# Kernel optimization log

Measured on AMD Instinct MI355X. Metric: run time of the kernel, lower is better.

Reference implementation:

```python
import jax, jax.numpy as jnp
import numpy as np

TEMP = 0.05
ALPHA = 0.1
EPS = 1e-12


def setup_inputs() -> dict:
    key = jax.random.key(0)
    k1, k2, k3, k4 = jax.random.split(key, 4)
    bs, emb_dim, n_class, n_aux = 16384, 512, 2000, 5
    features = jax.random.normal(k1, (bs, emb_dim), dtype=jnp.float32)
    word_embed = jax.random.normal(k2, (n_class, emb_dim), dtype=jnp.float32)
    label = jax.random.randint(k3, (bs,), 0, n_class)
    aux = jax.random.randint(k4, (bs, n_aux), 0, n_class)
    return {"features": features, "word_embed": word_embed, "label": label, "aux": aux}


def _cosine_logits(features, word_embed):
    # F.normalize(x, dim=-1): x / max(||x||, eps)
    f = features / jnp.maximum(jnp.linalg.norm(features, axis=-1, keepdims=True), EPS)
    w = word_embed / jnp.maximum(jnp.linalg.norm(word_embed, axis=-1, keepdims=True), EPS)
    return jnp.matmul(f, w.T) / TEMP  # (bs, n_class)


def reference(features, word_embed, label, aux):
    pred = _cosine_logits(features, word_embed)
    lse = jax.nn.logsumexp(pred, axis=1)                                  # log sum exp per row
    tgt = jnp.take_along_axis(pred, label[:, None], axis=1)[:, 0]         # pred[i, target[i]]
    # normal cross entropy: mean_i(-pred[i,t_i] + log sum exp(pred[i]))
    loss_normal = jnp.mean(-tgt + lse)
    # label-smoothing CE: -(1-a)*pred[i,t_i] + lse - (a/n_aux)*sum_j pred[i, aux[i,j]]
    single_alpha = ALPHA / aux.shape[-1]
    aux_logits = jnp.take_along_axis(pred, aux, axis=1)                   # (bs, n_aux)
    loss_ls = jnp.mean(-(1.0 - ALPHA) * tgt + lse - single_alpha * jnp.sum(aux_logits, axis=1))
    loss = 0.5 * (loss_normal + loss_ls)
    acc = jnp.mean((jnp.argmax(pred, axis=1) == label).astype(jnp.float32))
    return loss, acc
```

## Files before the change

kernel.cpp:

```cpp
#include <hip/hip_runtime.h>
#include <hip/hip_bf16.h>
#include <stdint.h>

#define BS   16384
#define NC   2000
#define NCP  2048
#define EMB  512
#define NAUX 5
#define NCHUNK 32
#define GBLK 4096

typedef __bf16 bf16x8 __attribute__((ext_vector_type(8)));
typedef float  f32x4  __attribute__((ext_vector_type(4)));

__global__ __launch_bounds__(256) void norm_kernel(
    const float* __restrict__ feat, const float* __restrict__ wemb,
    __bf16* __restrict__ fn, __bf16* __restrict__ wn)
{
    const int sub = threadIdx.x & 15;
    const int row = blockIdx.x * 16 + (threadIdx.x >> 4);

    if (row >= BS + NC) {
        bf16x8 z = {};
        bf16x8* d = (bf16x8*)(wn + (size_t)(row - BS) * EMB) + sub * 4;
        #pragma unroll
        for (int i = 0; i < 4; ++i) d[i] = z;
        return;
    }
    const float* src;
    __bf16* dst;
    if (row < BS) { src = feat + (size_t)row * EMB;        dst = fn + (size_t)row * EMB; }
    else          { src = wemb + (size_t)(row - BS) * EMB; dst = wn + (size_t)(row - BS) * EMB; }

    const float4* s4 = (const float4*)src + sub * 8;
    float4 x[8];
    float ss = 0.f;
    #pragma unroll
    for (int i = 0; i < 8; ++i) {
        x[i] = s4[i];
        ss += x[i].x * x[i].x + x[i].y * x[i].y + x[i].z * x[i].z + x[i].w * x[i].w;
    }
    #pragma unroll
    for (int m = 1; m < 16; m <<= 1) ss += __shfl_xor(ss, m, 64);
    const float scale = 1.0f / fmaxf(sqrtf(ss), 1e-12f);

    bf16x8* d = (bf16x8*)dst + sub * 4;
    #pragma unroll
    for (int i = 0; i < 4; ++i) {
        bf16x8 o;
        o[0] = (__bf16)(x[2*i].x   * scale); o[1] = (__bf16)(x[2*i].y   * scale);
        o[2] = (__bf16)(x[2*i].z   * scale); o[3] = (__bf16)(x[2*i].w   * scale);
        o[4] = (__bf16)(x[2*i+1].x * scale); o[5] = (__bf16)(x[2*i+1].y * scale);
        o[6] = (__bf16)(x[2*i+1].z * scale); o[7] = (__bf16)(x[2*i+1].w * scale);
        d[i] = o;
    }
}

__global__ __launch_bounds__(256) void main_kernel(
    const __bf16* __restrict__ fn, const __bf16* __restrict__ wn,
    float* __restrict__ es_p, unsigned* __restrict__ key_p)
{
    __shared__ __align__(16) __bf16 As[128 * 64];
    __shared__ __align__(16) __bf16 Bs[128 * 64];

    const int tid   = threadIdx.x;
    const int lane  = tid & 63;
    const int l15   = lane & 15;
    const int quad  = lane >> 4;
    const int wv    = tid >> 6;
    const int wvM   = wv >> 1;
    const int wvN   = wv & 1;
    const int xcd   = blockIdx.x & 7;
    const int j     = blockIdx.x >> 3;
    const int mTile = xcd * 16 + (j >> 4);
    const int nTile = j & 15;

    const __bf16* fbase = fn + (size_t)mTile * 128 * EMB;
    const __bf16* wbase = wn + (size_t)nTile * 128 * EMB;

    const int sRowIn = lane >> 3;
    const int sChunk = (lane & 7) ^ sRowIn;
    f32x4 acc[4][4] = {};

    for (int kk = 0; kk < EMB; kk += 64) {
        __syncthreads();
        #pragma unroll
        for (int p = 0; p < 4; ++p) {
            const int slot = wv * 4 + p;
            const size_t goff = (size_t)(slot * 8 + sRowIn) * EMB + kk + sChunk * 8;
            __builtin_amdgcn_global_load_lds(
                (const __attribute__((address_space(1))) void*)(fbase + goff),
                (__attribute__((address_space(3))) void*)(As + slot * 512), 16, 0, 0);
            __builtin_amdgcn_global_load_lds(
                (const __attribute__((address_space(1))) void*)(wbase + goff),
                (__attribute__((address_space(3))) void*)(Bs + slot * 512), 16, 0, 0);
        }
        __builtin_amdgcn_s_waitcnt(0);
        __syncthreads();

        #pragma unroll
        for (int kc = 0; kc < 2; ++kc) {
            bf16x8 aF[4], bF[4];
            #pragma unroll
            for (int i = 0; i < 4; ++i) {
                const int ar = wvM * 64 + i * 16 + l15;
                const int br = wvN * 64 + i * 16 + l15;
                const int ca = ((kc * 4 + quad) ^ (ar & 7)) * 8;
                const int cb = ((kc * 4 + quad) ^ (br & 7)) * 8;
                aF[i] = *(const bf16x8*)(As + ar * 64 + ca);
                bF[i] = *(const bf16x8*)(Bs + br * 64 + cb);
            }
            #pragma unroll
            for (int mi = 0; mi < 4; ++mi)
                #pragma unroll
                for (int ni = 0; ni < 4; ++ni)
                    acc[mi][ni] = __builtin_amdgcn_mfma_f32_16x16x32_bf16(
                        aF[mi], bF[ni], acc[mi][ni], 0, 0, 0);
        }
    }

    const float C20 = 28.853900817779268f;
    const int chunk = nTile * 2 + wvN;
    #pragma unroll
    for (int mi = 0; mi < 4; ++mi) {
        float    es[4] = {0.f, 0.f, 0.f, 0.f};
        unsigned km[4] = {0u, 0u, 0u, 0u};
        #pragma unroll
        for (int ni = 0; ni < 4; ++ni) {
            const int col = nTile * 128 + wvN * 64 + ni * 16 + l15;
            const unsigned colenc = 2047u - (unsigned)col;
            const bool valid = (col < NC);
            #pragma unroll
            for (int r = 0; r < 4; ++r) {
                float v = valid ? acc[mi][ni][r] : -3.0f;
                es[r] += exp2f((v - 1.0f) * C20);
                unsigned u = __float_as_uint(v);
                unsigned k = u ^ (unsigned)(((int)u >> 31) | 0x80000000);
                unsigned pk = (k & 0xFFFFF800u) | colenc;
                km[r] = pk > km[r] ? pk : km[r];
            }
        }
        #pragma unroll
        for (int r = 0; r < 4; ++r) {
            #pragma unroll
            for (int m = 1; m < 16; m <<= 1) {
                es[r] += __shfl_xor(es[r], m, 64);
                unsigned x = __shfl_xor(km[r], m, 64);
                km[r] = x > km[r] ? x : km[r];
            }
        }
        if (l15 == 0) {
            #pragma unroll
            for (int r = 0; r < 4; ++r) {
                const int row = mTile * 128 + wvM * 64 + mi * 16 + quad * 4 + r;
                es_p [(size_t)row * NCHUNK + chunk] = es[r];
                key_p[(size_t)row * NCHUNK + chunk] = km[r];
            }
        }
    }
}

__global__ __launch_bounds__(256) void gather_fin_kernel(
    const __bf16* __restrict__ fn, const __bf16* __restrict__ wn,
    const int* __restrict__ label, const int* __restrict__ aux,
    const float* __restrict__ es_p, const unsigned* __restrict__ key_p,
    float* __restrict__ blkpart)
{
    const int lane = threadIdx.x & 63;
    const int wv   = threadIdx.x >> 6;
    const int row  = blockIdx.x * 4 + wv;

    bf16x8 f8 = *((const bf16x8*)fn + (size_t)row * (EMB / 8) + lane);
    float fv[8];
    #pragma unroll
    for (int j = 0; j < 8; ++j) fv[j] = (float)f8[j];

    const int lab = label[row];
    int cols[6];
    cols[0] = lab;
    #pragma unroll
    for (int j = 0; j < NAUX; ++j) cols[j + 1] = aux[row * NAUX + j];

    float res[6];
    #pragma unroll
    for (int c = 0; c < 6; ++c) {
        bf16x8 w8 = *((const bf16x8*)wn + (size_t)cols[c] * (EMB / 8) + lane);
        float d = 0.f;
        #pragma unroll
        for (int j = 0; j < 8; ++j) d += fv[j] * (float)w8[j];
        #pragma unroll
        for (int m = 1; m < 64; m <<= 1) d += __shfl_xor(d, m, 64);
        res[c] = d;
    }
    const float tgt  = res[0] * 20.0f;
    const float auxs = (res[1] + res[2] + res[3] + res[4] + res[5]) * 20.0f;

    const int c = lane & 31;
    float    es = es_p [(size_t)row * NCHUNK + c];
    unsigned k  = key_p[(size_t)row * NCHUNK + c];
    #pragma unroll
    for (int m = 1; m < 32; m <<= 1) {
        es += __shfl_xor(es, m, 64);
        unsigned x = __shfl_xor(k, m, 64);
        k = x > k ? x : k;
    }
    const int amax = 2047 - (int)(k & 0x7FFu);
    const float loss = 20.0f + logf(es) - 0.95f * tgt - 0.01f * auxs;
    const float acc  = (amax == lab) ? 1.0f : 0.0f;

    __shared__ float sl[4], sa[4];
    if (lane == 0) { sl[wv] = loss; sa[wv] = acc; }
    __syncthreads();
    if (threadIdx.x == 0) {
        blkpart[blockIdx.x]        = sl[0] + sl[1] + sl[2] + sl[3];
        blkpart[GBLK + blockIdx.x] = sa[0] + sa[1] + sa[2] + sa[3];
    }
}

__global__ __launch_bounds__(256) void fin2_kernel(
    const float* __restrict__ blkpart, float* __restrict__ out)
{
    float l = 0.f, a = 0.f;
    for (int i = threadIdx.x; i < GBLK; i += 256) {
        l += blkpart[i];
        a += blkpart[GBLK + i];
    }
    #pragma unroll
    for (int m = 1; m < 64; m <<= 1) {
        l += __shfl_xor(l, m, 64);
        a += __shfl_xor(a, m, 64);
    }
    __shared__ float sl[4], sa[4];
    const int wv = threadIdx.x >> 6;
    if ((threadIdx.x & 63) == 0) { sl[wv] = l; sa[wv] = a; }
    __syncthreads();
    if (threadIdx.x == 0) {
        out[0] = (sl[0] + sl[1] + sl[2] + sl[3]) / (float)BS;
        out[1] = (sa[0] + sa[1] + sa[2] + sa[3]) / (float)BS;
    }
}

extern "C" void kernel_launch(void* const* d_in, const int* in_sizes, int n_in,
                              void* d_out, int out_size, void* d_ws, size_t ws_size,
                              hipStream_t stream)
{
    const float* feat  = (const float*)d_in[0];
    const float* wemb  = (const float*)d_in[1];
    const int*   label = (const int*)d_in[2];
    const int*   aux   = (const int*)d_in[3];

    char* ws = (char*)d_ws;
    __bf16*   fn      = (__bf16*)(ws);
    __bf16*   wn      = (__bf16*)(ws + 16777216);
    float*    es_p    = (float*)(ws + 18874368);
    unsigned* key_p   = (unsigned*)(ws + 20971520);
    float*    blkpart = (float*)(ws + 23068672);
    float*    out     = (float*)d_out;

    hipLaunchKernelGGL(norm_kernel, dim3((BS + NCP) / 16), dim3(256), 0, stream,
                       feat, wemb, fn, wn);
    hipLaunchKernelGGL(main_kernel, dim3((BS / 128) * (NCP / 128)), dim3(256), 0, stream,
                       fn, wn, es_p, key_p);
    hipLaunchKernelGGL(gather_fin_kernel, dim3(GBLK), dim3(256), 0, stream,
                       fn, wn, label, aux, es_p, key_p, blkpart);
    hipLaunchKernelGGL(fin2_kernel, dim3(1), dim3(256), 0, stream, blkpart, out);
}
```

Measured before the change: 160.2 us.

## Run cosine-logit GEMM in fp8 e4m3 with bf16 copies kept for gathers

The norm kernel now emits both fp8 e4m3 and bf16 normalized rows. The main GEMM loads fp8 tiles (256-byte K chunks, two stages) into LDS and uses the fp8 MFMA, halving operand bytes. The target/aux gather still uses bf16. This adds extra writes in the norm kernel and a larger LDS footprint, and fp8 rounding at temperature 0.05 risks perturbing argmax and logsumexp.

After: 148.7 us. 7.2% less time.

```diff
diff --git a/kernel.cpp b/kernel.cpp
--- a/kernel.cpp
+++ b/kernel.cpp
@@ -1,5 +1,6 @@
 #include <hip/hip_runtime.h>
 #include <hip/hip_bf16.h>
+#include <hip/hip_fp8.h>
 #include <stdint.h>
 
 #define BS   16384
@@ -15,22 +16,30 @@
 
 __global__ __launch_bounds__(256) void norm_kernel(
     const float* __restrict__ feat, const float* __restrict__ wemb,
-    __bf16* __restrict__ fn, __bf16* __restrict__ wn)
+    unsigned char* __restrict__ fn8, unsigned char* __restrict__ wn8,
+    __bf16* __restrict__ fnb, __bf16* __restrict__ wnb)
 {
     const int sub = threadIdx.x & 15;
     const int row = blockIdx.x * 16 + (threadIdx.x >> 4);
 
     if (row >= BS + NC) {
+        const int pr = row - BS;
+        uint4 z4 = {0, 0, 0, 0};
+        ((uint4*)(wn8 + (size_t)pr * EMB))[sub * 2]     = z4;
+        ((uint4*)(wn8 + (size_t)pr * EMB))[sub * 2 + 1] = z4;
         bf16x8 z = {};
-        bf16x8* d = (bf16x8*)(wn + (size_t)(row - BS) * EMB) + sub * 4;
+        bf16x8* d = (bf16x8*)(wnb + (size_t)pr * EMB) + sub * 4;
         #pragma unroll
         for (int i = 0; i < 4; ++i) d[i] = z;
         return;
     }
     const float* src;
-    __bf16* dst;
-    if (row < BS) { src = feat + (size_t)row * EMB;        dst = fn + (size_t)row * EMB; }
-    else          { src = wemb + (size_t)(row - BS) * EMB; dst = wn + (size_t)(row - BS) * EMB; }
+    unsigned char* dst8;
+    __bf16* dstb;
+    if (row < BS) { src = feat + (size_t)row * EMB;
+                    dst8 = fn8 + (size_t)row * EMB;        dstb = fnb + (size_t)row * EMB; }
+    else          { src = wemb + (size_t)(row - BS) * EMB;
+                    dst8 = wn8 + (size_t)(row - BS) * EMB; dstb = wnb + (size_t)(row - BS) * EMB; }
 
     const float4* s4 = (const float4*)src + sub * 8;
     float4 x[8];
@@ -44,24 +53,35 @@
     for (int m = 1; m < 16; m <<= 1) ss += __shfl_xor(ss, m, 64);
     const float scale = 1.0f / fmaxf(sqrtf(ss), 1e-12f);
 
-    bf16x8* d = (bf16x8*)dst + sub * 4;
+    float v[32];
+    #pragma unroll
+    for (int i = 0; i < 8; ++i) {
+        v[4*i]   = x[i].x * scale; v[4*i+1] = x[i].y * scale;
+        v[4*i+2] = x[i].z * scale; v[4*i+3] = x[i].w * scale;
+    }
+    bf16x8* db = (bf16x8*)dstb + sub * 4;
     #pragma unroll
     for (int i = 0; i < 4; ++i) {
         bf16x8 o;
-        o[0] = (__bf16)(x[2*i].x   * scale); o[1] = (__bf16)(x[2*i].y   * scale);
-        o[2] = (__bf16)(x[2*i].z   * scale); o[3] = (__bf16)(x[2*i].w   * scale);
-        o[4] = (__bf16)(x[2*i+1].x * scale); o[5] = (__bf16)(x[2*i+1].y * scale);
-        o[6] = (__bf16)(x[2*i+1].z * scale); o[7] = (__bf16)(x[2*i+1].w * scale);
-        d[i] = o;
-    }
+        #pragma unroll
+        for (int jj = 0; jj < 8; ++jj) o[jj] = (__bf16)v[8*i + jj];
+        db[i] = o;
+    }
+    unsigned char pb[32];
+    #pragma unroll
+    for (int i = 0; i < 32; ++i)
+        pb[i] = __hip_cvt_float_to_fp8(v[i], __HIP_SATFINITE, __HIP_E4M3);
+    uint4* d8 = (uint4*)(dst8 + sub * 32);
+    d8[0] = *(const uint4*)(pb);
+    d8[1] = *(const uint4*)(pb + 16);
 }
 
 __global__ __launch_bounds__(256) void main_kernel(
-    const __bf16* __restrict__ fn, const __bf16* __restrict__ wn,
+    const unsigned char* __restrict__ fn8, const unsigned char* __restrict__ wn8,
     float* __restrict__ es_p, unsigned* __restrict__ key_p)
 {
-    __shared__ __align__(16) __bf16 As[128 * 64];
-    __shared__ __align__(16) __bf16 Bs[128 * 64];
+    __shared__ __align__(16) unsigned char As[128 * 256];
+    __shared__ __align__(16) unsigned char Bs[128 * 256];
 
     const int tid   = threadIdx.x;
     const int lane  = tid & 63;
@@ -75,46 +95,50 @@
     const int mTile = xcd * 16 + (j >> 4);
     const int nTile = j & 15;
 
-    const __bf16* fbase = fn + (size_t)mTile * 128 * EMB;
-    const __bf16* wbase = wn + (size_t)nTile * 128 * EMB;
-
-    const int sRowIn = lane >> 3;
-    const int sChunk = (lane & 7) ^ sRowIn;
+    const unsigned char* fbase = fn8 + (size_t)mTile * 128 * EMB;
+    const unsigned char* wbase = wn8 + (size_t)nTile * 128 * EMB;
+
+    const int rIn = lane >> 4;
+    const int cPh = lane & 15;
     f32x4 acc[4][4] = {};
 
-    for (int kk = 0; kk < EMB; kk += 64) {
+    #pragma unroll
+    for (int kk = 0; kk < 2; ++kk) {
         __syncthreads();
         #pragma unroll
-        for (int p = 0; p < 4; ++p) {
-            const int slot = wv * 4 + p;
-            const size_t goff = (size_t)(slot * 8 + sRowIn) * EMB + kk + sChunk * 8;
+        for (int p = 0; p < 8; ++p) {
+            const int slot = wv * 8 + p;
+            const int row  = slot * 4 + rIn;
+            const int cLog = cPh ^ (row & 7);
+            const size_t goff = (size_t)row * EMB + kk * 256 + cLog * 16;
             __builtin_amdgcn_global_load_lds(
                 (const __attribute__((address_space(1))) void*)(fbase + goff),
-                (__attribute__((address_space(3))) void*)(As + slot * 512), 16, 0, 0);
+                (__attribute__((address_space(3))) void*)(As + slot * 1024), 16, 0, 0);
             __builtin_amdgcn_global_load_lds(
                 (const __attribute__((address_space(1))) void*)(wbase + goff),
-                (__attribute__((address_space(3))) void*)(Bs + slot * 512), 16, 0, 0);
+                (__attribute__((address_space(3))) void*)(Bs + slot * 1024), 16, 0, 0);
         }
         __builtin_amdgcn_s_waitcnt(0);
         __syncthreads();
 
         #pragma unroll
-        for (int kc = 0; kc < 2; ++kc) {
-            bf16x8 aF[4], bF[4];
+        for (int kc = 0; kc < 8; ++kc) {
+            long aF[4], bF[4];
+            const int c16  = kc * 2 + (quad >> 1);
+            const int hoff = (quad & 1) << 3;
             #pragma unroll
             for (int i = 0; i < 4; ++i) {
                 const int ar = wvM * 64 + i * 16 + l15;
                 const int br = wvN * 64 + i * 16 + l15;
-                const int ca = ((kc * 4 + quad) ^ (ar & 7)) * 8;
-                const int cb = ((kc * 4 + quad) ^ (br & 7)) * 8;
-                aF[i] = *(const bf16x8*)(As + ar * 64 + ca);
-                bF[i] = *(const bf16x8*)(Bs + br * 64 + cb);
+                const int ca = ((c16 ^ (l15 & 7)) << 4) + hoff;
+                aF[i] = *(const long*)(As + ar * 256 + ca);
+                bF[i] = *(const long*)(Bs + br * 256 + ca);
             }
             #pragma unroll
             for (int mi = 0; mi < 4; ++mi)
                 #pragma unroll
                 for (int ni = 0; ni < 4; ++ni)
-                    acc[mi][ni] = __builtin_amdgcn_mfma_f32_16x16x32_bf16(
+                    acc[mi][ni] = __builtin_amdgcn_mfma_f32_16x16x32_fp8_fp8(
                         aF[mi], bF[ni], acc[mi][ni], 0, 0, 0);
         }
     }
@@ -161,7 +185,7 @@
 }
 
 __global__ __launch_bounds__(256) void gather_fin_kernel(
-    const __bf16* __restrict__ fn, const __bf16* __restrict__ wn,
+    const __bf16* __restrict__ fnb, const __bf16* __restrict__ wnb,
     const int* __restrict__ label, const int* __restrict__ aux,
     const float* __restrict__ es_p, const unsigned* __restrict__ key_p,
     float* __restrict__ blkpart)
@@ -170,7 +194,7 @@
     const int wv   = threadIdx.x >> 6;
     const int row  = blockIdx.x * 4 + wv;
 
-    bf16x8 f8 = *((const bf16x8*)fn + (size_t)row * (EMB / 8) + lane);
+    bf16x8 f8 = *((const bf16x8*)fnb + (size_t)row * (EMB / 8) + lane);
     float fv[8];
     #pragma unroll
     for (int j = 0; j < 8; ++j) fv[j] = (float)f8[j];
@@ -184,7 +208,7 @@
     float res[6];
     #pragma unroll
     for (int c = 0; c < 6; ++c) {
-        bf16x8 w8 = *((const bf16x8*)wn + (size_t)cols[c] * (EMB / 8) + lane);
+        bf16x8 w8 = *((const bf16x8*)wnb + (size_t)cols[c] * (EMB / 8) + lane);
         float d = 0.f;
         #pragma unroll
         for (int j = 0; j < 8; ++j) d += fv[j] * (float)w8[j];
@@ -250,18 +274,20 @@
     const int*   aux   = (const int*)d_in[3];
 
     char* ws = (char*)d_ws;
-    __bf16*   fn      = (__bf16*)(ws);
-    __bf16*   wn      = (__bf16*)(ws + 16777216);
-    float*    es_p    = (float*)(ws + 18874368);
-    unsigned* key_p   = (unsigned*)(ws + 20971520);
-    float*    blkpart = (float*)(ws + 23068672);
-    float*    out     = (float*)d_out;
+    unsigned char* fn8     = (unsigned char*)(ws);
+    unsigned char* wn8     = (unsigned char*)(ws + 8388608);
+    __bf16*        fnb     = (__bf16*)(ws + 9437184);
+    __bf16*        wnb     = (__bf16*)(ws + 26214400);
+    float*         es_p    = (float*)(ws + 28311552);
+    unsigned*      key_p   = (unsigned*)(ws + 30408704);
+    float*         blkpart = (float*)(ws + 32505856);
+    float*         out     = (float*)d_out;
 
     hipLaunchKernelGGL(norm_kernel, dim3((BS + NCP) / 16), dim3(256), 0, stream,
-                       feat, wemb, fn, wn);
+                       feat, wemb, fn8, wn8, fnb, wnb);
     hipLaunchKernelGGL(main_kernel, dim3((BS / 128) * (NCP / 128)), dim3(256), 0, stream,
-                       fn, wn, es_p, key_p);
+                       fn8, wn8, es_p, key_p);
     hipLaunchKernelGGL(gather_fin_kernel, dim3(GBLK), dim3(256), 0, stream,
-                       fn, wn, label, aux, es_p, key_p, blkpart);
+                       fnb, wnb, label, aux, es_p, key_p, blkpart);
     hipLaunchKernelGGL(fin2_kernel, dim3(1), dim3(256), 0, stream, blkpart, out);
 }
```
